# Kernel optimization log

Measured on AMD Instinct MI355X. Metric: run time of the kernel, lower is better.

Reference implementation:

```python
import jax, jax.numpy as jnp
import numpy as np

SAMPLING_FACTOR = 4

def setup_inputs() -> dict:
    key = jax.random.key(0)
    x = jax.random.normal(key, (8, 8192, 512), dtype=jnp.float32)
    return {"x": x}

def reference(x) -> jnp.ndarray:
    # Causal 'avg' pooling: output[i] = mean(x[:, :(i+1)*sf, :]) over time axis.
    # O(L) rewrite of the original O(L^2) loop: prefix cumsum + strided gather.
    B, L, D = x.shape
    sf = SAMPLING_FACTOR
    out_len = L // sf
    csum = jnp.cumsum(x, axis=1)                       # (B, L, D) prefix sums
    idx = jnp.arange(1, out_len + 1) * sf - 1          # end positions (i+1)*sf - 1
    gathered = csum[:, idx, :]                          # (B, out_len, D)
    counts = (idx + 1).astype(x.dtype)[None, :, None]   # window lengths
    return gathered / counts
```

## Files before the change

### kernel.cpp

```cpp
#include <hip/hip_runtime.h>


#define BB   8
#define LL   8192
#define DD4  128
#define NC   128
#define CL   (LL / NC)
#define OPC  (CL / 4)
#define OL   (LL / 4)

typedef float vf4 __attribute__((ext_vector_type(4)));

__global__ __launch_bounds__(256) void ds_phase1(const vf4* __restrict__ x,
                                                 vf4* __restrict__ sums,
                                                 vf4* __restrict__ out) {
    int tid = blockIdx.x * blockDim.x + threadIdx.x;
    int d4 = tid & (DD4 - 1);
    int c  = (tid >> 7) & (NC - 1);
    int b  = tid >> 14;

    const vf4* p = x + (((size_t)b * LL + c * CL) * DD4 + d4);
    vf4* o = out + (((size_t)b * OL + c * OPC) * DD4 + d4);

    vf4 s = (vf4)0.f;
    #pragma unroll
    for (int j = 0; j < CL; j += 8) {
        vf4 v0 = __builtin_nontemporal_load(&p[(j + 0) * DD4]);
        vf4 v1 = __builtin_nontemporal_load(&p[(j + 1) * DD4]);
        vf4 v2 = __builtin_nontemporal_load(&p[(j + 2) * DD4]);
        vf4 v3 = __builtin_nontemporal_load(&p[(j + 3) * DD4]);
        vf4 v4 = __builtin_nontemporal_load(&p[(j + 4) * DD4]);
        vf4 v5 = __builtin_nontemporal_load(&p[(j + 5) * DD4]);
        vf4 v6 = __builtin_nontemporal_load(&p[(j + 6) * DD4]);
        vf4 v7 = __builtin_nontemporal_load(&p[(j + 7) * DD4]);
        s += v0 + v1 + v2 + v3;
        o[((j >> 2) + 0) * DD4] = s;
        s += v4 + v5 + v6 + v7;
        o[((j >> 2) + 1) * DD4] = s;
    }
    sums[(b * NC + c) * DD4 + d4] = s;
}

__global__ __launch_bounds__(256) void ds_phase2(vf4* __restrict__ out,
                                                 const vf4* __restrict__ sums) {
    int tid = blockIdx.x * blockDim.x + threadIdx.x;
    int d4 = tid & (DD4 - 1);
    int c  = (tid >> 7) & (NC - 1);
    int b  = tid >> 14;

    vf4* o = out + (((size_t)b * OL + c * OPC) * DD4 + d4);

    vf4 v[OPC];
    #pragma unroll
    for (int k = 0; k < OPC; ++k) v[k] = o[(size_t)k * DD4];

    vf4 r = (vf4)0.f;
    const vf4* sp = sums + b * NC * DD4 + d4;
    #pragma unroll 4
    for (int q = 0; q < c; ++q) r += sp[q * DD4];

    const int base = c * CL;
    #pragma unroll
    for (int k = 0; k < OPC; ++k) {
        const float inv = 1.0f / (float)(base + 4 * k + 4);
        o[(size_t)k * DD4] = (v[k] + r) * inv;
    }
}

extern "C" void kernel_launch(void* const* d_in, const int* in_sizes, int n_in,
                              void* d_out, int out_size, void* d_ws, size_t ws_size,
                              hipStream_t stream) {
    const vf4* x = (const vf4*)d_in[0];
    vf4* out = (vf4*)d_out;
    vf4* sums = (vf4*)d_ws;

    const int total = BB * NC * DD4;
    const int block = 256;
    const int grid  = total / block;

    ds_phase1<<<grid, block, 0, stream>>>(x, sums, out);
    ds_phase2<<<grid, block, 0, stream>>>(out, sums);
}
```

Before: 205.7 us.

## Fuse two-phase scan into one kernel with grid-wide atomic barrier

Merges the two scan passes into one kernel. Each thread keeps its 16 running partial sums in registers, then all blocks wait on a software grid barrier (an atomic counter in workspace, reset by a memset) before adding the carry from earlier chunks and writing the output once with nontemporal stores. This removes the write and re-read of the intermediate output and one kernel launch. In exchange it needs all 512 blocks resident at once to avoid deadlock, and adds a memset plus barrier spin latency.

```diff
diff --git a/kernel.cpp b/kernel.cpp
--- a/kernel.cpp
+++ b/kernel.cpp
@@ -8,20 +8,23 @@
 #define CL   (LL / NC)
 #define OPC  (CL / 4)
 #define OL   (LL / 4)
+#define NBLK 512
+#define SUMS_BYTES ((size_t)BB * NC * DD4 * 16)
 
 typedef float vf4 __attribute__((ext_vector_type(4)));
 
-__global__ __launch_bounds__(256) void ds_phase1(const vf4* __restrict__ x,
-                                                 vf4* __restrict__ sums,
-                                                 vf4* __restrict__ out) {
-    int tid = blockIdx.x * blockDim.x + threadIdx.x;
-    int d4 = tid & (DD4 - 1);
-    int c  = (tid >> 7) & (NC - 1);
-    int b  = tid >> 14;
+__global__ __launch_bounds__(256) void ds_fused(const vf4* __restrict__ x,
+                                                vf4* __restrict__ sums,
+                                                unsigned int* __restrict__ cnt,
+                                                vf4* __restrict__ out) {
+    const int tid = blockIdx.x * blockDim.x + threadIdx.x;
+    const int d4 = tid & (DD4 - 1);
+    const int c  = (tid >> 7) & (NC - 1);
+    const int b  = tid >> 14;
 
     const vf4* p = x + (((size_t)b * LL + c * CL) * DD4 + d4);
-    vf4* o = out + (((size_t)b * OL + c * OPC) * DD4 + d4);
 
+    vf4 v[OPC];
     vf4 s = (vf4)0.f;
     #pragma unroll
     for (int j = 0; j < CL; j += 8) {
@@ -34,36 +37,40 @@
         vf4 v6 = __builtin_nontemporal_load(&p[(j + 6) * DD4]);
         vf4 v7 = __builtin_nontemporal_load(&p[(j + 7) * DD4]);
         s += v0 + v1 + v2 + v3;
-        o[((j >> 2) + 0) * DD4] = s;
+        v[(j >> 2) + 0] = s;
         s += v4 + v5 + v6 + v7;
-        o[((j >> 2) + 1) * DD4] = s;
+        v[(j >> 2) + 1] = s;
     }
     sums[(b * NC + c) * DD4 + d4] = s;
-}
 
-__global__ __launch_bounds__(256) void ds_phase2(vf4* __restrict__ out,
-                                                 const vf4* __restrict__ sums) {
-    int tid = blockIdx.x * blockDim.x + threadIdx.x;
-    int d4 = tid & (DD4 - 1);
-    int c  = (tid >> 7) & (NC - 1);
-    int b  = tid >> 14;
+    __syncthreads();
+    if (threadIdx.x == 0) {
+        __threadfence();
+        __hip_atomic_fetch_add(cnt, 1u, __ATOMIC_RELEASE, __HIP_MEMORY_SCOPE_AGENT);
+        while (__hip_atomic_load(cnt, __ATOMIC_RELAXED, __HIP_MEMORY_SCOPE_AGENT) < NBLK)
+            __builtin_amdgcn_s_sleep(8);
+        __threadfence();
+    }
+    __syncthreads();
+
+    vf4 r0 = (vf4)0.f, r1 = (vf4)0.f, r2 = (vf4)0.f, r3 = (vf4)0.f;
+    const vf4* sp = sums + b * NC * DD4 + d4;
+    int q = 0;
+    for (; q + 4 <= c; q += 4) {
+        r0 += sp[(q + 0) * DD4];
+        r1 += sp[(q + 1) * DD4];
+        r2 += sp[(q + 2) * DD4];
+        r3 += sp[(q + 3) * DD4];
+    }
+    for (; q < c; ++q) r0 += sp[q * DD4];
+    const vf4 r = (r0 + r1) + (r2 + r3);
 
     vf4* o = out + (((size_t)b * OL + c * OPC) * DD4 + d4);
-
-    vf4 v[OPC];
-    #pragma unroll
-    for (int k = 0; k < OPC; ++k) v[k] = o[(size_t)k * DD4];
-
-    vf4 r = (vf4)0.f;
-    const vf4* sp = sums + b * NC * DD4 + d4;
-    #pragma unroll 4
-    for (int q = 0; q < c; ++q) r += sp[q * DD4];
-
     const int base = c * CL;
     #pragma unroll
     for (int k = 0; k < OPC; ++k) {
         const float inv = 1.0f / (float)(base + 4 * k + 4);
-        o[(size_t)k * DD4] = (v[k] + r) * inv;
+        __builtin_nontemporal_store((v[k] + r) * inv, &o[(size_t)k * DD4]);
     }
 }
 
@@ -73,11 +80,8 @@
     const vf4* x = (const vf4*)d_in[0];
     vf4* out = (vf4*)d_out;
     vf4* sums = (vf4*)d_ws;
+    unsigned int* cnt = (unsigned int*)((char*)d_ws + SUMS_BYTES);
 
-    const int total = BB * NC * DD4;
-    const int block = 256;
-    const int grid  = total / block;
-
-    ds_phase1<<<grid, block, 0, stream>>>(x, sums, out);
-    ds_phase2<<<grid, block, 0, stream>>>(out, sums);
+    hipMemsetAsync(cnt, 0, 64, stream);
+    ds_fused<<<NBLK, 256, 0, stream>>>(x, sums, cnt, out);
 }
```

Result: slower. 265.2 us (+28.9%).
